# Optimization experiments

Measured on AMD Instinct MI355X. Metric: run time of the kernel, lower is better.

The kernel has to match this reference:

```python
import jax, jax.numpy as jnp
import numpy as np

NUM_HEADS = 16  # matches init_kwargs num_heads
ROPE_BASE = 10000.0


def _rope(x):
    # x: [B, H, T, d_k]; canonical interleaved rotary embedding
    d = x.shape[-1]
    T = x.shape[-2]
    inv_freq = 1.0 / (ROPE_BASE ** (jnp.arange(0, d, 2, dtype=jnp.float32) / d))  # [d/2]
    ang = jnp.arange(T, dtype=jnp.float32)[:, None] * inv_freq[None, :]  # [T, d/2]
    cos, sin = jnp.cos(ang), jnp.sin(ang)  # broadcast over B,H
    x1 = x[..., 0::2]
    x2 = x[..., 1::2]
    even = x1 * cos - x2 * sin
    odd = x1 * sin + x2 * cos
    return jnp.stack([even, odd], axis=-1).reshape(x.shape)


def setup_inputs() -> dict:
    key = jax.random.key(0)
    ks = jax.random.split(key, 5)
    B, T, D = 2, 2048, 2048
    s = 1.0 / np.sqrt(D)
    return {
        "x": jax.random.normal(ks[0], (B, T, D), dtype=jnp.float32),
        "Wkqv": jax.random.normal(ks[1], (D, 3 * D), dtype=jnp.float32) * s,
        "bkqv": jax.random.normal(ks[2], (3 * D,), dtype=jnp.float32) * 0.01,
        "Wo": jax.random.normal(ks[3], (D, D), dtype=jnp.float32) * s,
        "bo": jax.random.normal(ks[4], (D,), dtype=jnp.float32) * 0.01,
    }


def reference(x, Wkqv, bkqv, Wo, bo):
    B, T, D = x.shape
    H = NUM_HEADS
    d_k = D // H
    kqv = x @ Wkqv + bkqv  # [B, T, 3D]
    # split order per source: index 0 = K, 1 = Q, 2 = V
    k, q, v = jnp.split(kqv, 3, axis=-1)

    def heads(t):  # [B, T, D] -> [B, H, T, d_k]
        return t.reshape(B, T, H, d_k).transpose(0, 2, 1, 3)

    k, q, v = heads(k), heads(q), heads(v)
    k = _rope(k)
    q = _rope(q)
    scores = jnp.einsum('bhtd,bhTd->bhtT', q, k)  # [B, H, T, T]
    causal = jnp.triu(jnp.ones((T, T), dtype=bool), k=1)
    scores = jnp.where(causal, -jnp.inf, scores)
    attn = jax.nn.softmax(scores / jnp.sqrt(jnp.float32(d_k)), axis=-1)
    out = jnp.einsum('bhtT,bhTd->bhtd', attn, v)  # [B, H, T, d_k]
    out = out.transpose(0, 2, 1, 3).reshape(B, T, D)
    return out @ Wo + bo
```

## Files before the change

### kernel.cpp

```cpp
#include <hip/hip_runtime.h>
#include <cstdint>
#include <cstddef>

typedef __attribute__((ext_vector_type(4))) float  floatx4;
typedef __attribute__((ext_vector_type(8))) __bf16 bf16x8;
typedef __attribute__((ext_vector_type(4))) __bf16 bf16x4;

#define B_   2
#define T_   2048
#define D_   2048
#define H_   16
#define DK   128
#define BT_  (B_ * T_)
#define N3   (3 * D_)

__device__ __forceinline__ void async_copy16(const void* g, void* l) {
    __builtin_amdgcn_global_load_lds((const __attribute__((address_space(1))) void*)g,
                                     (__attribute__((address_space(3))) void*)l,
                                     16, 0, 0);
}

__global__ void cast_bf16_kernel(const float* __restrict__ in, __bf16* __restrict__ out, int n4) {
    int i = blockIdx.x * 256 + threadIdx.x;
    if (i >= n4) return;
    float4 v = ((const float4*)in)[i];
    bf16x4 o;
    o.x = (__bf16)v.x; o.y = (__bf16)v.y; o.z = (__bf16)v.z; o.w = (__bf16)v.w;
    ((bf16x4*)out)[i] = o;
}

__global__ void transcast_kernel(const float* __restrict__ in, __bf16* __restrict__ out, int R, int C) {
    __shared__ float tile[32][33];
    int c0 = blockIdx.x * 32, r0 = blockIdx.y * 32;
    int tx = threadIdx.x, ty = threadIdx.y;
#pragma unroll
    for (int j = 0; j < 32; j += 8)
        tile[ty + j][tx] = in[(size_t)(r0 + ty + j) * C + c0 + tx];
    __syncthreads();
#pragma unroll
    for (int j = 0; j < 32; j += 8)
        out[(size_t)(c0 + ty + j) * R + r0 + tx] = (__bf16)tile[tx][ty + j];
}

template <typename OutT>
__global__ __launch_bounds__(256)
void gemm_bt(const __bf16* __restrict__ A, const __bf16* __restrict__ BTm,
             const float* __restrict__ bias, OutT* __restrict__ C,
             int M, int N, int K) {
    __shared__ __align__(16) __bf16 As[128 * 64];
    __shared__ __align__(16) __bf16 Bs[128 * 64];
    const int tid  = threadIdx.x;
    const int lane = tid & 63;
    const int wave = tid >> 6;
    const int quad = lane >> 4;
    const int l16  = lane & 15;
    const int m0 = blockIdx.y * 128;
    const int n0 = blockIdx.x * 128;
    const int wm = (wave & 1) * 64;
    const int wn = (wave >> 1) * 64;

    const floatx4 z4 = {0.f, 0.f, 0.f, 0.f};
    floatx4 acc[4][4];
#pragma unroll
    for (int i = 0; i < 4; ++i)
#pragma unroll
        for (int j = 0; j < 4; ++j) acc[i][j] = z4;

    int           sOff[4];
    const __bf16* gA[4];
    const __bf16* gB[4];
#pragma unroll
    for (int i = 0; i < 4; ++i) {
        int s = i * 256 + tid;
        int row = s >> 3, cs = s & 7;
        int gc = cs ^ (row & 7);
        sOff[i] = s * 8;
        gA[i] = A   + (size_t)(m0 + row) * K + gc * 8;
        gB[i] = BTm + (size_t)(n0 + row) * K + gc * 8;
    }

    for (int kt = 0; kt < K; kt += 64) {
        __syncthreads();
#pragma unroll
        for (int i = 0; i < 4; ++i) {
            async_copy16(gA[i] + kt, As + sOff[i]);
            async_copy16(gB[i] + kt, Bs + sOff[i]);
        }
        __syncthreads();
#pragma unroll
        for (int ks2 = 0; ks2 < 2; ++ks2) {
            bf16x8 af[4], bf[4];
#pragma unroll
            for (int t = 0; t < 4; ++t) {
                int rowA = wm + t * 16 + l16;
                int ca = (ks2 * 4 + quad) ^ (rowA & 7);
                af[t] = *(const bf16x8*)(As + rowA * 64 + ca * 8);
                int rowB = wn + t * 16 + l16;
                int cb = (ks2 * 4 + quad) ^ (rowB & 7);
                bf[t] = *(const bf16x8*)(Bs + rowB * 64 + cb * 8);
            }
#pragma unroll
            for (int mt = 0; mt < 4; ++mt)
#pragma unroll
                for (int nt = 0; nt < 4; ++nt)
                    acc[mt][nt] = __builtin_amdgcn_mfma_f32_16x16x32_bf16(af[mt], bf[nt], acc[mt][nt], 0, 0, 0);
        }
    }

#pragma unroll
    for (int nt = 0; nt < 4; ++nt) {
        int n = n0 + wn + nt * 16 + l16;
        float bv = bias[n];
#pragma unroll
        for (int mt = 0; mt < 4; ++mt)
#pragma unroll
            for (int r = 0; r < 4; ++r) {
                int m = m0 + wm + mt * 16 + quad * 4 + r;
                C[(size_t)m * N + n] = (OutT)(acc[mt][nt][r] + bv);
            }
    }
}

__global__ __launch_bounds__(256)
void gemm_kqv(const __bf16* __restrict__ A, const __bf16* __restrict__ BTm,
              const float* __restrict__ bias,
              __bf16* __restrict__ Kh, __bf16* __restrict__ Qh,
              __bf16* __restrict__ VT,
              int M, int N, int K) {
    __shared__ __align__(16) __bf16 smem[128 * 136];
    __bf16* As = smem;
    __bf16* Bs = smem + 128 * 64;
    const int tid  = threadIdx.x;
    const int lane = tid & 63;
    const int wave = tid >> 6;
    const int quad = lane >> 4;
    const int l16  = lane & 15;
    const int m0 = blockIdx.y * 128;
    const int n0 = blockIdx.x * 128;
    const int wm = (wave & 1) * 64;
    const int wn = (wave >> 1) * 64;

    const floatx4 z4 = {0.f, 0.f, 0.f, 0.f};
    floatx4 acc[4][4];
#pragma unroll
    for (int i = 0; i < 4; ++i)
#pragma unroll
        for (int j = 0; j < 4; ++j) acc[i][j] = z4;

    int           sOff[4];
    const __bf16* gA[4];
    const __bf16* gB[4];
#pragma unroll
    for (int i = 0; i < 4; ++i) {
        int s = i * 256 + tid;
        int row = s >> 3, cs = s & 7;
        int gc = cs ^ (row & 7);
        sOff[i] = s * 8;
        gA[i] = A   + (size_t)(m0 + row) * K + gc * 8;
        gB[i] = BTm + (size_t)(n0 + row) * K + gc * 8;
    }

    for (int kt = 0; kt < K; kt += 64) {
        __syncthreads();
#pragma unroll
        for (int i = 0; i < 4; ++i) {
            async_copy16(gA[i] + kt, As + sOff[i]);
            async_copy16(gB[i] + kt, Bs + sOff[i]);
        }
        __syncthreads();
#pragma unroll
        for (int ks2 = 0; ks2 < 2; ++ks2) {
            bf16x8 af[4], bf[4];
#pragma unroll
            for (int t = 0; t < 4; ++t) {
                int rowA = wm + t * 16 + l16;
                int ca = (ks2 * 4 + quad) ^ (rowA & 7);
                af[t] = *(const bf16x8*)(As + rowA * 64 + ca * 8);
                int rowB = wn + t * 16 + l16;
                int cb = (ks2 * 4 + quad) ^ (rowB & 7);
                bf[t] = *(const bf16x8*)(Bs + rowB * 64 + cb * 8);
            }
#pragma unroll
            for (int mt = 0; mt < 4; ++mt)
#pragma unroll
                for (int nt = 0; nt < 4; ++nt)
                    acc[mt][nt] = __builtin_amdgcn_mfma_f32_16x16x32_bf16(af[mt], bf[nt], acc[mt][nt], 0, 0, 0);
        }
    }

    const int which = n0 >> 11;
    const int h  = (n0 & (D_ - 1)) >> 7;
    const int b  = m0 >> 11;
    const int t0 = m0 & (T_ - 1);
    const int bh = b * H_ + h;

    if (which == 2) {
        __syncthreads();
#pragma unroll
        for (int nt = 0; nt < 4; ++nt) {
            const int n  = n0 + wn + nt * 16 + l16;
            const float bv = bias[n];
            const int dd = wn + nt * 16 + l16;
#pragma unroll
            for (int mt = 0; mt < 4; ++mt)
#pragma unroll
                for (int r = 0; r < 4; ++r) {
                    const int tl = wm + mt * 16 + quad * 4 + r;
                    smem[dd * 136 + tl] = (__bf16)(acc[mt][nt][r] + bv);
                }
        }
        __syncthreads();
#pragma unroll
        for (int i = 0; i < 8; ++i) {
            int s = i * 256 + tid;
            int dd = s >> 4, c = s & 15;
            bf16x8 vv = *(const bf16x8*)(smem + dd * 136 + c * 8);
            *(bf16x8*)(VT + ((size_t)bh * DK + dd) * T_ + t0 + c * 8) = vv;
        }
    } else {
        const float qscale = which ? 0.12751740f : 1.0f;
        __bf16* dst = which ? Qh : Kh;
#pragma unroll
        for (int nt = 0; nt < 4; ++nt) {
            const int n  = n0 + wn + nt * 16 + l16;
            const float bv = bias[n];
            const int dd = wn + nt * 16 + l16;
            const float freq_rev = 0.15915494309189535f *
                exp2f((float)(dd >> 1) * (-13.287712379549449f / 64.f));
#pragma unroll
            for (int mt = 0; mt < 4; ++mt)
#pragma unroll
                for (int r = 0; r < 4; ++r) {
                    const int t = t0 + wm + mt * 16 + quad * 4 + r;
                    const float val = acc[mt][nt][r] + bv;
                    const float other = __shfl_xor(val, 1);
                    const float x1 = (dd & 1) ? other : val;
                    const float x2 = (dd & 1) ? val : other;
                    float rev = (float)t * freq_rev;
                    rev -= floorf(rev);
                    const float ang = rev * 6.283185307179586f;
                    const float sn = __sinf(ang), cn = __cosf(ang);
                    const float res = (dd & 1) ? (x1 * sn + x2 * cn)
                                               : (x1 * cn - x2 * sn);
                    dst[((size_t)bh * T_ + t) * DK + dd] = (__bf16)(res * qscale);
                }
        }
    }
}

__global__ __launch_bounds__(256)
void fa_kernel(const __bf16* __restrict__ Qg, const __bf16* __restrict__ Kg,
               const __bf16* __restrict__ VTg, __bf16* __restrict__ Og) {
    __shared__ __align__(16) __bf16 Ks[2][64 * 128];
    __shared__ __align__(16) __bf16 Vs[2][128 * 64];
    __shared__ __align__(16) __bf16 Ps[4][16 * 64];
    const int tid  = threadIdx.x;
    const int lane = tid & 63, wave = tid >> 6;
    const int quad = lane >> 4, l16 = lane & 15;
    const int bh = blockIdx.y;
    const int j  = blockIdx.x;
    const int b = bh >> 4, h = bh & 15;

    const __bf16* Kb = Kg  + (size_t)bh * T_ * DK;
    const __bf16* Vb = VTg + (size_t)bh * DK * T_;
    __bf16* Psw = Ps[wave];
    const int swzP = (l16 & 7) << 1;

    const floatx4 z4 = {0.f, 0.f, 0.f, 0.f};

    int           sK[4], sV[4];
    const __bf16* gK[4];
    const __bf16* gV[4];
#pragma unroll
    for (int i = 0; i < 4; ++i) {
        int s = i * 256 + tid;
        { int row = s >> 4, cs = s & 15; int gc = cs ^ (row & 7);
          sK[i] = s * 8; gK[i] = Kb + (size_t)row * DK + gc * 8; }
        { int row = s >> 3, cs = s & 7;  int gc = cs ^ (row & 7);
          sV[i] = s * 8; gV[i] = Vb + (size_t)row * T_ + gc * 8; }
    }

    for (int half = 0; half < 2; ++half) {
        const int qt = half ? (31 - j) : j;
        const int q0 = qt * 64;
        const int qpos = q0 + wave * 16 + l16;

        __syncthreads();
        {
            const __bf16* Qb = Qg + (size_t)(bh * T_ + q0) * DK;
#pragma unroll
            for (int i = 0; i < 4; ++i) {
                int s = i * 256 + tid;
                int row = s >> 4, cs = s & 15;
                int gc = cs ^ (row & 7);
                async_copy16(Qb + row * DK + gc * 8, &Ks[0][0] + s * 8);
            }
        }
        __syncthreads();
        bf16x8 qf[4];
#pragma unroll
        for (int ks = 0; ks < 4; ++ks) {
            int row = wave * 16 + l16;
            int c = (ks * 4 + quad) ^ (row & 7);
            qf[ks] = *(const bf16x8*)(&Ks[0][0] + row * DK + c * 8);
        }
        __syncthreads();

#pragma unroll
        for (int i = 0; i < 4; ++i) async_copy16(gK[i], &Ks[0][0] + sK[i]);
#pragma unroll
        for (int i = 0; i < 4; ++i) async_copy16(gV[i], &Vs[0][0] + sV[i]);

        float m_i = -1e30f, l_i = 0.f;
        floatx4 accO[8];
#pragma unroll
        for (int dt = 0; dt < 8; ++dt) accO[dt] = z4;

        for (int kt = 0; kt <= qt; ++kt) {
            const int cur = kt & 1;
            if (kt < qt) {
                const int nb = cur ^ 1;
                const size_t koff = (size_t)(kt + 1) * 64 * DK;
                const size_t voff = (size_t)(kt + 1) * 64;
#pragma unroll
                for (int i = 0; i < 4; ++i) async_copy16(gK[i] + koff, &Ks[nb][0] + sK[i]);
#pragma unroll
                for (int i = 0; i < 4; ++i) async_copy16(gV[i] + voff, &Vs[nb][0] + sV[i]);
                asm volatile("s_waitcnt vmcnt(8)" ::: "memory");
            } else {
                asm volatile("s_waitcnt vmcnt(0)" ::: "memory");
            }
            __builtin_amdgcn_s_barrier();

            const __bf16* Kcur = &Ks[cur][0];
            const __bf16* Vcur = &Vs[cur][0];

            floatx4 sc[4];
#pragma unroll
            for (int nt = 0; nt < 4; ++nt) sc[nt] = z4;
            __builtin_amdgcn_s_setprio(1);
#pragma unroll
            for (int ks = 0; ks < 4; ++ks)
#pragma unroll
                for (int nt = 0; nt < 4; ++nt) {
                    int row = nt * 16 + l16;
                    int c = (ks * 4 + quad) ^ (row & 7);
                    bf16x8 kf = *(const bf16x8*)(Kcur + row * DK + c * 8);
                    sc[nt] = __builtin_amdgcn_mfma_f32_16x16x32_bf16(kf, qf[ks], sc[nt], 0, 0, 0);
                }
            __builtin_amdgcn_s_setprio(0);

            float mnew = -1e30f;
            if (kt == qt) {
#pragma unroll
                for (int nt = 0; nt < 4; ++nt) {
                    int kbase = kt * 64 + nt * 16 + quad * 4;
#pragma unroll
                    for (int r = 0; r < 4; ++r) {
                        float v = sc[nt][r];
                        v = (kbase + r > qpos) ? -1e30f : v;
                        sc[nt][r] = v;
                        mnew = fmaxf(mnew, v);
                    }
                }
            } else {
#pragma unroll
                for (int nt = 0; nt < 4; ++nt)
#pragma unroll
                    for (int r = 0; r < 4; ++r) mnew = fmaxf(mnew, sc[nt][r]);
            }
            mnew = fmaxf(mnew, __shfl_xor(mnew, 16));
            mnew = fmaxf(mnew, __shfl_xor(mnew, 32));
            const float mi = fmaxf(m_i, mnew);
            const float alpha = exp2f(m_i - mi);
            m_i = mi;

            float rs = 0.f;
#pragma unroll
            for (int nt = 0; nt < 4; ++nt)
#pragma unroll
                for (int r = 0; r < 4; ++r) {
                    float pv = exp2f(sc[nt][r] - mi);
                    sc[nt][r] = pv;
                    rs += pv;
                }
            rs += __shfl_xor(rs, 16);
            rs += __shfl_xor(rs, 32);
            l_i = l_i * alpha + rs;
#pragma unroll
            for (int dt = 0; dt < 8; ++dt)
#pragma unroll
                for (int r = 0; r < 4; ++r) accO[dt][r] *= alpha;

#pragma unroll
            for (int nt = 0; nt < 4; ++nt) {
                bf16x4 pw;
                pw.x = (__bf16)sc[nt][0]; pw.y = (__bf16)sc[nt][1];
                pw.z = (__bf16)sc[nt][2]; pw.w = (__bf16)sc[nt][3];
                int g = (nt * 4 + quad) ^ swzP;
                *(bf16x4*)(Psw + l16 * 64 + g * 4) = pw;
            }
            __builtin_amdgcn_s_setprio(1);
#pragma unroll
            for (int kc = 0; kc < 2; ++kc) {
                int gk = (kc * 8 + quad * 2) ^ swzP;
                bf16x8 pb = *(const bf16x8*)(Psw + l16 * 64 + gk * 4);
#pragma unroll
                for (int dt = 0; dt < 8; ++dt) {
                    int vrow = dt * 16 + l16;
                    int vch = (kc * 4 + quad) ^ (vrow & 7);
                    bf16x8 vf = *(const bf16x8*)(Vcur + vrow * 64 + vch * 8);
                    accO[dt] = __builtin_amdgcn_mfma_f32_16x16x32_bf16(vf, pb, accO[dt], 0, 0, 0);
                }
            }
            __builtin_amdgcn_s_setprio(0);

            __builtin_amdgcn_s_barrier();
        }

        const float inv = 1.0f / l_i;
        __bf16* orow = Og + (size_t)(b * T_ + qpos) * D_ + h * DK;
#pragma unroll
        for (int dt = 0; dt < 8; ++dt) {
            bf16x4 ow;
            ow.x = (__bf16)(accO[dt][0] * inv);
            ow.y = (__bf16)(accO[dt][1] * inv);
            ow.z = (__bf16)(accO[dt][2] * inv);
            ow.w = (__bf16)(accO[dt][3] * inv);
            *(bf16x4*)(orow + dt * 16 + quad * 4) = ow;
        }
    }
}

extern "C" void kernel_launch(void* const* d_in, const int* in_sizes, int n_in,
                              void* d_out, int out_size, void* d_ws, size_t ws_size,
                              hipStream_t stream) {
    const float* x    = (const float*)d_in[0];
    const float* Wkqv = (const float*)d_in[1];
    const float* bkqv = (const float*)d_in[2];
    const float* Wo   = (const float*)d_in[3];
    const float* bo   = (const float*)d_in[4];
    float* out = (float*)d_out;

    char* p = (char*)d_ws;
    __bf16* xb    = (__bf16*)p; p += (size_t)BT_ * D_ * 2;
    __bf16* WkqvT = (__bf16*)p; p += (size_t)D_ * N3 * 2;
    __bf16* WoT   = (__bf16*)p; p += (size_t)D_ * D_ * 2;
    __bf16* qh    = (__bf16*)p; p += (size_t)BT_ * D_ * 2;
    __bf16* kh    = (__bf16*)p; p += (size_t)BT_ * D_ * 2;
    __bf16* vT    = (__bf16*)p; p += (size_t)BT_ * D_ * 2;
    __bf16* ao    = (__bf16*)p; p += (size_t)BT_ * D_ * 2;

    cast_bf16_kernel<<<(BT_ * D_ / 4 + 255) / 256, 256, 0, stream>>>(x, xb, BT_ * D_ / 4);
    transcast_kernel<<<dim3(N3 / 32, D_ / 32), dim3(32, 8), 0, stream>>>(Wkqv, WkqvT, D_, N3);
    transcast_kernel<<<dim3(D_ / 32, D_ / 32), dim3(32, 8), 0, stream>>>(Wo, WoT, D_, D_);
    gemm_kqv<<<dim3(N3 / 128, BT_ / 128), 256, 0, stream>>>(xb, WkqvT, bkqv, kh, qh, vT, BT_, N3, D_);
    fa_kernel<<<dim3(16, B_ * H_), 256, 0, stream>>>(qh, kh, vT, ao);
    gemm_bt<float><<<dim3(D_ / 128, BT_ / 128), 256, 0, stream>>>(ao, WoT, bo, out, BT_, D_, D_);
}
```

Baseline: 397.3 us.

## Use 128-row query tiles with 8 waves in attention and vectorize weight transpose

The attention kernel now runs 512 threads (8 waves) per block over 128-query tiles, so each staged K/V tile is shared by twice as many query rows and the grid halves to 8x32 blocks. The causal mask now applies to the last two key tiles. The weight transpose-cast kernel is rewritten with 64x64 tiles, float4 loads and 16-byte bf16 stores to cut per-element memory traffic. Trade-offs are fewer blocks on the GPU (256 total), which may lower occupancy and load balance, and some wasted work on fully masked key tiles for the early waves.

After: 402.2 us. About the same (+1.2%).

```diff
diff --git a/kernel.cpp b/kernel.cpp
--- a/kernel.cpp
+++ b/kernel.cpp
@@ -29,17 +29,29 @@
     ((bf16x4*)out)[i] = o;
 }
 
-__global__ void transcast_kernel(const float* __restrict__ in, __bf16* __restrict__ out, int R, int C) {
-    __shared__ float tile[32][33];
-    int c0 = blockIdx.x * 32, r0 = blockIdx.y * 32;
-    int tx = threadIdx.x, ty = threadIdx.y;
-#pragma unroll
-    for (int j = 0; j < 32; j += 8)
-        tile[ty + j][tx] = in[(size_t)(r0 + ty + j) * C + c0 + tx];
+__global__ __launch_bounds__(256)
+void transcast_kernel(const float* __restrict__ in, __bf16* __restrict__ out, int R, int C) {
+    __shared__ float tile[64][65];
+    const int tid = threadIdx.x;
+    const int r0 = blockIdx.y * 64, c0 = blockIdx.x * 64;
+#pragma unroll
+    for (int p = 0; p < 4; ++p) {
+        int u = p * 256 + tid;
+        int r = u >> 4, c4 = (u & 15) * 4;
+        float4 v = *(const float4*)(in + (size_t)(r0 + r) * C + c0 + c4);
+        tile[r][c4 + 0] = v.x; tile[r][c4 + 1] = v.y;
+        tile[r][c4 + 2] = v.z; tile[r][c4 + 3] = v.w;
+    }
     __syncthreads();
 #pragma unroll
-    for (int j = 0; j < 32; j += 8)
-        out[(size_t)(c0 + ty + j) * R + r0 + tx] = (__bf16)tile[tx][ty + j];
+    for (int p = 0; p < 2; ++p) {
+        int v = p * 256 + tid;
+        int cc = v >> 3, rr = (v & 7) * 8;
+        bf16x8 o;
+#pragma unroll
+        for (int i2 = 0; i2 < 8; ++i2) o[i2] = (__bf16)tile[rr + i2][cc];
+        *(bf16x8*)(out + (size_t)(c0 + cc) * R + r0 + rr) = o;
+    }
 }
 
 template <typename OutT>
@@ -248,12 +260,12 @@
     }
 }
 
-__global__ __launch_bounds__(256)
+__global__ __launch_bounds__(512)
 void fa_kernel(const __bf16* __restrict__ Qg, const __bf16* __restrict__ Kg,
                const __bf16* __restrict__ VTg, __bf16* __restrict__ Og) {
     __shared__ __align__(16) __bf16 Ks[2][64 * 128];
     __shared__ __align__(16) __bf16 Vs[2][128 * 64];
-    __shared__ __align__(16) __bf16 Ps[4][16 * 64];
+    __shared__ __align__(16) __bf16 Ps[8][16 * 64];
     const int tid  = threadIdx.x;
     const int lane = tid & 63, wave = tid >> 6;
     const int quad = lane >> 4, l16 = lane & 15;
@@ -268,12 +280,12 @@
 
     const floatx4 z4 = {0.f, 0.f, 0.f, 0.f};
 
-    int           sK[4], sV[4];
-    const __bf16* gK[4];
-    const __bf16* gV[4];
-#pragma unroll
-    for (int i = 0; i < 4; ++i) {
-        int s = i * 256 + tid;
+    int           sK[2], sV[2];
+    const __bf16* gK[2];
+    const __bf16* gV[2];
+#pragma unroll
+    for (int i = 0; i < 2; ++i) {
+        int s = i * 512 + tid;
         { int row = s >> 4, cs = s & 15; int gc = cs ^ (row & 7);
           sK[i] = s * 8; gK[i] = Kb + (size_t)row * DK + gc * 8; }
         { int row = s >> 3, cs = s & 7;  int gc = cs ^ (row & 7);
@@ -281,16 +293,17 @@
     }
 
     for (int half = 0; half < 2; ++half) {
-        const int qt = half ? (31 - j) : j;
-        const int q0 = qt * 64;
+        const int qt = half ? (15 - j) : j;
+        const int q0 = qt * 128;
         const int qpos = q0 + wave * 16 + l16;
+        const int nkt = 2 * qt + 2;
 
         __syncthreads();
         {
             const __bf16* Qb = Qg + (size_t)(bh * T_ + q0) * DK;
 #pragma unroll
             for (int i = 0; i < 4; ++i) {
-                int s = i * 256 + tid;
+                int s = i * 512 + tid;
                 int row = s >> 4, cs = s & 15;
                 int gc = cs ^ (row & 7);
                 async_copy16(Qb + row * DK + gc * 8, &Ks[0][0] + s * 8);
@@ -307,26 +320,26 @@
         __syncthreads();
 
 #pragma unroll
-        for (int i = 0; i < 4; ++i) async_copy16(gK[i], &Ks[0][0] + sK[i]);
-#pragma unroll
-        for (int i = 0; i < 4; ++i) async_copy16(gV[i], &Vs[0][0] + sV[i]);
+        for (int i = 0; i < 2; ++i) async_copy16(gK[i], &Ks[0][0] + sK[i]);
+#pragma unroll
+        for (int i = 0; i < 2; ++i) async_copy16(gV[i], &Vs[0][0] + sV[i]);
 
         float m_i = -1e30f, l_i = 0.f;
         floatx4 accO[8];
 #pragma unroll
         for (int dt = 0; dt < 8; ++dt) accO[dt] = z4;
 
-        for (int kt = 0; kt <= qt; ++kt) {
+        for (int kt = 0; kt < nkt; ++kt) {
             const int cur = kt & 1;
-            if (kt < qt) {
+            if (kt < nkt - 1) {
                 const int nb = cur ^ 1;
                 const size_t koff = (size_t)(kt + 1) * 64 * DK;
                 const size_t voff = (size_t)(kt + 1) * 64;
 #pragma unroll
-                for (int i = 0; i < 4; ++i) async_copy16(gK[i] + koff, &Ks[nb][0] + sK[i]);
-#pragma unroll
-                for (int i = 0; i < 4; ++i) async_copy16(gV[i] + voff, &Vs[nb][0] + sV[i]);
-                asm volatile("s_waitcnt vmcnt(8)" ::: "memory");
+                for (int i = 0; i < 2; ++i) async_copy16(gK[i] + koff, &Ks[nb][0] + sK[i]);
+#pragma unroll
+                for (int i = 0; i < 2; ++i) async_copy16(gV[i] + voff, &Vs[nb][0] + sV[i]);
+                asm volatile("s_waitcnt vmcnt(4)" ::: "memory");
             } else {
                 asm volatile("s_waitcnt vmcnt(0)" ::: "memory");
             }
@@ -351,7 +364,7 @@
             __builtin_amdgcn_s_setprio(0);
 
             float mnew = -1e30f;
-            if (kt == qt) {
+            if (kt >= 2 * qt) {
 #pragma unroll
                 for (int nt = 0; nt < 4; ++nt) {
                     int kbase = kt * 64 + nt * 16 + quad * 4;
@@ -452,9 +465,9 @@
     __bf16* ao    = (__bf16*)p; p += (size_t)BT_ * D_ * 2;
 
     cast_bf16_kernel<<<(BT_ * D_ / 4 + 255) / 256, 256, 0, stream>>>(x, xb, BT_ * D_ / 4);
-    transcast_kernel<<<dim3(N3 / 32, D_ / 32), dim3(32, 8), 0, stream>>>(Wkqv, WkqvT, D_, N3);
-    transcast_kernel<<<dim3(D_ / 32, D_ / 32), dim3(32, 8), 0, stream>>>(Wo, WoT, D_, D_);
+    transcast_kernel<<<dim3(N3 / 64, D_ / 64), 256, 0, stream>>>(Wkqv, WkqvT, D_, N3);
+    transcast_kernel<<<dim3(D_ / 64, D_ / 64), 256, 0, stream>>>(Wo, WoT, D_, D_);
     gemm_kqv<<<dim3(N3 / 128, BT_ / 128), 256, 0, stream>>>(xb, WkqvT, bkqv, kh, qh, vT, BT_, N3, D_);
-    fa_kernel<<<dim3(16, B_ * H_), 256, 0, stream>>>(qh, kh, vT, ao);
+    fa_kernel<<<dim3(8, B_ * H_), 512, 0, stream>>>(qh, kh, vT, ao);
     gemm_bt<float><<<dim3(D_ / 128, BT_ / 128), 256, 0, stream>>>(ao, WoT, bo, out, BT_, D_, D_);
 }
```
